# Performance work log

Hardware: AMD Instinct MI355X
Metric: run time of the kernel (lower is better)

Reference implementation:

```python
import jax, jax.numpy as jnp
import numpy as np

N_U = 100000   # num 'u' nodes
N_V = 100000   # num 'v' nodes (destination type)
D = 128        # feature dim
E1 = 3200000   # edges ('u','r1','v')
E2 = 3200000   # edges ('v','r2','v')


def setup_inputs() -> dict:
    key = jax.random.key(0)
    ks = jax.random.split(key, 10)
    inv = 1.0 / np.sqrt(D)
    inv3 = 1.0 / np.sqrt(3 * D)
    return {
        "x_u": jax.random.normal(ks[0], (N_U, D), jnp.float32),
        "x_v": jax.random.normal(ks[1], (N_V, D), jnp.float32),
        "W_r1": jax.random.normal(ks[2], (D, D), jnp.float32) * inv,
        "W_r2": jax.random.normal(ks[3], (D, D), jnp.float32) * inv,
        "W_gate": jax.random.normal(ks[4], (3 * D, 3 * D), jnp.float32) * inv3,
        "b_gate": jnp.zeros((3 * D,), jnp.float32),
        "W_aggr": jax.random.normal(ks[5], (3 * D, D), jnp.float32) * inv3,
        "b_aggr": jnp.zeros((D,), jnp.float32),
        "edge_index_r1": jax.random.randint(ks[6], (2, E1), 0, N_V, dtype=jnp.int64),
        "edge_index_r2": jax.random.randint(ks[7], (2, E2), 0, N_V, dtype=jnp.int64),
    }


def reference(x_u, x_v, W_r1, W_r2, W_gate, b_gate, W_aggr, b_aggr,
              edge_index_r1, edge_index_r2):
    n_v = x_v.shape[0]
    # per-edge-type conv: gather source features, per-relation linear message
    msg1 = x_u[edge_index_r1[0]] @ W_r1   # [E1, D]
    msg2 = x_v[edge_index_r2[0]] @ W_r2   # [E2, D]
    # concat all relations targeting dst 'v' (as in out_dict concatenation)
    msg = jnp.concatenate([msg1, msg2], axis=0)              # [E1+E2, D]
    idx = jnp.concatenate([edge_index_r1[1], edge_index_r2[1]])  # [E1+E2]
    # sum aggregation (scatter_add into zeros of shape [N_v, D])
    s = jax.ops.segment_sum(msg, idx, num_segments=n_v)
    # mean = sum / count.clamp(min=1)
    cnt = jax.ops.segment_sum(jnp.ones_like(msg), idx, num_segments=n_v)
    mean = s / jnp.clip(cnt, 1.0)
    # max with include_self=True over zero-initialized output -> max(msgs, 0), empty rows = 0
    mx = jnp.maximum(jax.ops.segment_max(msg, idx, num_segments=n_v), 0.0)
    total = jnp.concatenate([s, mean, mx], axis=1)           # [N_v, 3D]
    mask = jnp.sum(jnp.abs(total), axis=1) == 0              # untouched nodes
    gate = jax.nn.sigmoid(total @ W_gate + b_gate)           # attention gate
    out = (total * gate) @ W_aggr + b_aggr                   # [N_v, D]
    return jnp.where(mask[:, None], 0.0, out)
```

## Files before the change

### kernel.cpp

```cpp
#include <hip/hip_runtime.h>
#include <math.h>

#define N_U 100000
#define N_V 100000
#define D 128
#define E1 3200000
#define E2 3200000
#define ETOT (E1 + E2)

#define NBUCK 196
#define SLACK 35000
#define PCHUNK 4096

typedef __bf16 bf16x8 __attribute__((ext_vector_type(8)));
typedef float f32x4 __attribute__((ext_vector_type(4)));

__device__ __forceinline__ unsigned short f2b(float f) {
  union { float f; unsigned int u; } v; v.f = f;
  unsigned int u = v.u;
  unsigned int r = u + 0x7fffu + ((u >> 16) & 1u);
  return (unsigned short)(r >> 16);
}
__device__ __forceinline__ float b2f(unsigned short s) {
  union { unsigned int u; float f; } v; v.u = ((unsigned int)s) << 16; return v.f;
}
__device__ __forceinline__ float b2f_lo(unsigned w) {
  union { unsigned u; float f; } v; v.u = w << 16; return v.f;
}
__device__ __forceinline__ float b2f_hi(unsigned w) {
  union { unsigned u; float f; } v; v.u = w & 0xffff0000u; return v.f;
}

__global__ void convert_w128(const float* __restrict__ W, unsigned short* __restrict__ WF) {
  int idx = blockIdx.x * 256 + threadIdx.x;
  if (idx < 128 * 128) {
    int k = idx >> 7, n = idx & 127;
    int f = (n >> 4) * 4 + (k >> 5);
    int out = f * 512 + ((n & 15) + 16 * ((k >> 3) & 3)) * 8 + (k & 7);
    WF[out] = f2b(W[k * 128 + n]);
  }
}
__global__ void convert_wg(const float* __restrict__ Wg, unsigned short* __restrict__ WgF) {
  int idx = blockIdx.x * 256 + threadIdx.x;
  if (idx < 384 * 384) {
    int k = idx / 384, n = idx - k * 384;
    int f = (n >> 4) * 12 + (k >> 5);
    int out = f * 512 + ((n & 15) + 16 * ((k >> 3) & 3)) * 8 + (k & 7);
    WgF[out] = f2b(Wg[k * 384 + n]);
  }
}
__global__ void convert_wa(const float* __restrict__ Wa, unsigned short* __restrict__ WaF) {
  int idx = blockIdx.x * 256 + threadIdx.x;
  if (idx < 384 * 128) {
    int k = idx >> 7, n = idx & 127;
    int f = (n >> 4) * 12 + (k >> 5);
    int out = f * 512 + ((n & 15) + 16 * ((k >> 3) & 3)) * 8 + (k & 7);
    WaF[out] = f2b(Wa[k * 128 + n]);
  }
}

#define LM 64
__global__ __launch_bounds__(256) void linear_mfma(
    const float* __restrict__ X, const unsigned short* __restrict__ WF,
    unsigned short* __restrict__ Hb, int nrows) {
  __shared__ unsigned short Xs[LM][136];
  const int t = threadIdx.x;
  const int row0 = blockIdx.x * LM;

  for (int i = t * 4; i < LM * 128; i += 1024) {
    int n = i >> 7, j = i & 127;
    int r = row0 + n;
    float4 v = make_float4(0.f, 0.f, 0.f, 0.f);
    if (r < nrows) v = *(const float4*)&X[(size_t)r * 128 + j];
    Xs[n][j] = f2b(v.x);
    Xs[n][j + 1] = f2b(v.y);
    Xs[n][j + 2] = f2b(v.z);
    Xs[n][j + 3] = f2b(v.w);
  }
  __syncthreads();

  const int wv = t >> 6;
  const int ln = t & 63;
  const int lr = ln & 15;
  const int lq = ln >> 4;
  const int m0 = wv * 16;

  bf16x8 a[4];
#pragma unroll
  for (int ks = 0; ks < 4; ks++)
    a[ks] = *(const bf16x8*)&Xs[m0 + lr][ks * 32 + lq * 8];

#pragma unroll
  for (int np = 0; np < 4; np++) {
    const int n0 = np * 32;
    f32x4 acc0 = {0.f, 0.f, 0.f, 0.f};
    f32x4 acc1 = {0.f, 0.f, 0.f, 0.f};
    const unsigned short* B0 = WF + (size_t)(np * 2) * 4 * 512 + ln * 8;
    const unsigned short* B1 = B0 + 4 * 512;
#pragma unroll
    for (int ks = 0; ks < 4; ks++) {
      bf16x8 b0 = *(const bf16x8*)(B0 + ks * 512);
      bf16x8 b1 = *(const bf16x8*)(B1 + ks * 512);
      acc0 = __builtin_amdgcn_mfma_f32_16x16x32_bf16(a[ks], b0, acc0, 0, 0, 0);
      acc1 = __builtin_amdgcn_mfma_f32_16x16x32_bf16(a[ks], b1, acc1, 0, 0, 0);
    }
#pragma unroll
    for (int r = 0; r < 4; r++) {
      int grow = row0 + m0 + lq * 4 + r;
      if (grow < nrows) {
        Hb[(size_t)grow * 128 + n0 + lr] = f2b(acc0[r]);
        Hb[(size_t)grow * 128 + n0 + 16 + lr] = f2b(acc1[r]);
      }
    }
  }
}

__global__ __launch_bounds__(256) void partition_kernel(
    const int* __restrict__ e1, const int* __restrict__ e2,
    int* __restrict__ bucketCursor, uint2* __restrict__ recs) {
  __shared__ int hist[256];
  __shared__ int scan_s[256];
  __shared__ int lstart[256];
  __shared__ int gbase[NBUCK];
  __shared__ int lcur[NBUCK];
  __shared__ uint2 buf[PCHUNK];

  const int t = threadIdx.x;
  const long base = (long)blockIdx.x * PCHUNK;
  const int n = (int)min((long)PCHUNK, (long)ETOT - base);

  hist[t] = 0;
  __syncthreads();

  uint2 myrec[PCHUNK / 256];
  int myb[PCHUNK / 256];
  int cnt = 0;
#pragma unroll
  for (int k = 0; k < PCHUNK / 256; k++) {
    int idx = t + k * 256;
    if (idx < n) {
      long i = base + idx;
      int enc, dst;
      if (i < E1) {
        dst = e1[E1 + i];
        enc = N_V + e1[i];
      } else {
        long j = i - E1;
        dst = e2[E2 + j];
        enc = e2[j];
      }
      myrec[cnt] = make_uint2((unsigned)enc, (unsigned)dst);
      int b = dst >> 9;
      myb[cnt] = b;
      atomicAdd(&hist[b], 1);
      cnt++;
    }
  }
  __syncthreads();

  int v = hist[t];
  scan_s[t] = v;
  __syncthreads();
  for (int off = 1; off < 256; off <<= 1) {
    int tmp = (t >= off) ? scan_s[t - off] : 0;
    __syncthreads();
    scan_s[t] += tmp;
    __syncthreads();
  }
  lstart[t] = scan_s[t] - v;
  if (t < NBUCK) {
    gbase[t] = atomicAdd(&bucketCursor[t], v);
    lcur[t] = scan_s[t] - v;
  }
  __syncthreads();

  for (int k = 0; k < cnt; k++) {
    int p = atomicAdd(&lcur[myb[k]], 1);
    buf[p] = myrec[k];
  }
  __syncthreads();

  for (int p = t; p < n; p += 256) {
    uint2 r = buf[p];
    int b = (int)(r.y >> 9);
    recs[(size_t)b * SLACK + gbase[b] + (p - lstart[b])] = r;
  }
}

__global__ __launch_bounds__(256) void bucket_scan(
    const int* __restrict__ bucketCnt, int* __restrict__ bucketBase) {
  __shared__ int s[256];
  const int t = threadIdx.x;
  int v = (t < NBUCK) ? bucketCnt[t] : 0;
  s[t] = v;
  __syncthreads();
  for (int off = 1; off < 256; off <<= 1) {
    int tmp = (t >= off) ? s[t - off] : 0;
    __syncthreads();
    s[t] += tmp;
    __syncthreads();
  }
  if (t < NBUCK) bucketBase[t] = s[t] - v;
  if (t == 255) bucketBase[NBUCK] = s[255];
}

__global__ __launch_bounds__(512) void bucket_fill(
    const uint2* __restrict__ recs, const int* __restrict__ bucketCnt,
    const int* __restrict__ bucketBase, int* __restrict__ row_ptr,
    int* __restrict__ col) {
  __shared__ int hist[512];
  __shared__ int s[512];
  __shared__ int curF[512];
  __shared__ int curB[512];
  const int t = threadIdx.x;
  const int b = blockIdx.x;
  const size_t slack = (size_t)b * SLACK;
  const int n = bucketCnt[b];
  const int outBase = bucketBase[b];
  const int n0 = b << 9;

  hist[t] = 0;
  __syncthreads();
  for (int p = t; p < n; p += 512)
    atomicAdd(&hist[recs[slack + p].y - n0], 1);
  __syncthreads();

  int v = hist[t];
  s[t] = v;
  __syncthreads();
  for (int off = 1; off < 512; off <<= 1) {
    int tmp = (t >= off) ? s[t - off] : 0;
    __syncthreads();
    s[t] += tmp;
    __syncthreads();
  }
  int excl = s[t] - v;
  curF[t] = excl;
  curB[t] = excl + v;
  int nd = n0 + t;
  if (nd < N_V) row_ptr[nd] = outBase + excl;
  if (b == 0 && t == 0) row_ptr[N_V] = ETOT;
  __syncthreads();

  for (int p = t; p < n; p += 512) {
    uint2 r = recs[slack + p];
    int local = r.y - n0;
    int q;
    if (r.x >= (unsigned)N_V) q = atomicSub(&curB[local], 1) - 1;
    else q = atomicAdd(&curF[local], 1);
    col[outBase + q] = (int)(r.x << 8);
  }
}

#define AGG1(w)                                        \
  do {                                                 \
    float lo = b2f_lo(w), hi = b2f_hi(w);              \
    s[2 * q] += lo; s[2 * q + 1] += hi;                \
    m[2 * q] = fmaxf(m[2 * q], lo);                    \
    m[2 * q + 1] = fmaxf(m[2 * q + 1], hi);            \
  } while (0)

__global__ __launch_bounds__(256) void aggregate_kernel(
    const unsigned short* __restrict__ Hb, const int* __restrict__ row_ptr,
    const int* __restrict__ col, unsigned int* __restrict__ SumB,
    unsigned int* __restrict__ MxB) {
  const int node = blockIdx.x * 4 + (threadIdx.x >> 6);
  const int lane = threadIdx.x & 63;
  const int grp = lane >> 4;
  const int fl = lane & 15;
  const int start = row_ptr[node];
  const int end = row_ptr[node + 1];
  const char* Hc = (const char*)Hb;
  const int byteoff = fl * 16;

  float s[8] = {0.f, 0.f, 0.f, 0.f, 0.f, 0.f, 0.f, 0.f};
  float m[8] = {0.f, 0.f, 0.f, 0.f, 0.f, 0.f, 0.f, 0.f};

  int i = start;
  for (; i + 31 < end; i += 32) {
    uint4 v[8];
#pragma unroll
    for (int g = 0; g < 8; g++) {
      int e = i + g * 4 + grp;
      v[g] = *(const uint4*)(Hc + (unsigned)col[e] + byteoff);
    }
#pragma unroll
    for (int g = 0; g < 8; g++) {
      { int q = 0; AGG1(v[g].x); }
      { int q = 1; AGG1(v[g].y); }
      { int q = 2; AGG1(v[g].z); }
      { int q = 3; AGG1(v[g].w); }
    }
  }
  for (; i < end; i += 4) {
    int e = i + grp;
    int ec = e < end ? e : (end - 1);
    uint4 v = *(const uint4*)(Hc + (unsigned)col[ec] + byteoff);
    if (e >= end) { v.x = 0u; v.y = 0u; v.z = 0u; v.w = 0u; }
    { int q = 0; AGG1(v.x); }
    { int q = 1; AGG1(v.y); }
    { int q = 2; AGG1(v.z); }
    { int q = 3; AGG1(v.w); }
  }

#pragma unroll
  for (int k = 0; k < 8; k++) {
    s[k] += __shfl_xor(s[k], 16, 64);
    m[k] = fmaxf(m[k], __shfl_xor(m[k], 16, 64));
    s[k] += __shfl_xor(s[k], 32, 64);
    m[k] = fmaxf(m[k], __shfl_xor(m[k], 32, 64));
  }

  if (lane < 16) {
    uint4 o;
    o.x = (unsigned)f2b(s[0]) | ((unsigned)f2b(s[1]) << 16);
    o.y = (unsigned)f2b(s[2]) | ((unsigned)f2b(s[3]) << 16);
    o.z = (unsigned)f2b(s[4]) | ((unsigned)f2b(s[5]) << 16);
    o.w = (unsigned)f2b(s[6]) | ((unsigned)f2b(s[7]) << 16);
    ((uint4*)SumB)[(size_t)node * 16 + fl] = o;
  } else if (lane < 32) {
    uint4 o;
    o.x = (unsigned)f2b(m[0]) | ((unsigned)f2b(m[1]) << 16);
    o.y = (unsigned)f2b(m[2]) | ((unsigned)f2b(m[3]) << 16);
    o.z = (unsigned)f2b(m[4]) | ((unsigned)f2b(m[5]) << 16);
    o.w = (unsigned)f2b(m[6]) | ((unsigned)f2b(m[7]) << 16);
    ((uint4*)MxB)[(size_t)node * 16 + fl] = o;
  }
}

#define EM 64
__global__ __launch_bounds__(256, 3) void epilogue_mfma(
    const unsigned short* __restrict__ SumB, const unsigned short* __restrict__ MxB,
    const int* __restrict__ row_ptr, const unsigned short* __restrict__ WgF,
    const float* __restrict__ bg, const unsigned short* __restrict__ WaF,
    const float* __restrict__ ba, float* __restrict__ Out) {
  __shared__ unsigned short Ts[EM][392];
  __shared__ float invs[EM];
  __shared__ int cnts[EM];

  const int t = threadIdx.x;
  const int node0 = blockIdx.x * EM;

  if (t < EM) {
    int nd = node0 + t;
    int c = 0;
    if (nd < N_V) c = row_ptr[nd + 1] - row_ptr[nd];
    cnts[t] = c;
    invs[t] = 1.0f / (float)(c > 0 ? c : 1);
  }
  __syncthreads();

  {
    const uint4* Sv = (const uint4*)SumB;
    const uint4* Mv = (const uint4*)MxB;
    for (int i = t; i < EM * 16; i += 256) {
      int n = i >> 4, u = i & 15;
      int nd = node0 + n;
      uint4 s = make_uint4(0u, 0u, 0u, 0u);
      uint4 m4 = make_uint4(0u, 0u, 0u, 0u);
      if (nd < N_V) {
        s = Sv[(size_t)nd * 16 + u];
        m4 = Mv[(size_t)nd * 16 + u];
      }
      float inv = invs[n];
      *(uint4*)&Ts[n][u * 8] = s;
      unsigned sw[4] = {s.x, s.y, s.z, s.w};
      unsigned mr[4];
#pragma unroll
      for (int q = 0; q < 4; q++) {
        unsigned short lo = f2b(b2f((unsigned short)sw[q]) * inv);
        unsigned short hi = f2b(b2f((unsigned short)(sw[q] >> 16)) * inv);
        mr[q] = (unsigned)lo | ((unsigned)hi << 16);
      }
      *(uint4*)&Ts[n][128 + u * 8] = make_uint4(mr[0], mr[1], mr[2], mr[3]);
      *(uint4*)&Ts[n][256 + u * 8] = m4;
    }
  }
  __syncthreads();

  const int wv = t >> 6;
  const int ln = t & 63;
  const int lr = ln & 15;
  const int lq = ln >> 4;

  f32x4 acc[4][6];
#pragma unroll
  for (int m = 0; m < 4; m++)
#pragma unroll
    for (int nt = 0; nt < 6; nt++) acc[m][nt] = (f32x4){0.f, 0.f, 0.f, 0.f};

  const unsigned short* Bg = WgF + (size_t)(wv * 6) * 12 * 512 + ln * 8;

#pragma unroll 2
  for (int kc = 0; kc < 12; kc++) {
    bf16x8 b[6];
#pragma unroll
    for (int nt = 0; nt < 6; nt++)
      b[nt] = *(const bf16x8*)(Bg + (nt * 12 + kc) * 512);
    bf16x8 a[4];
#pragma unroll
    for (int m = 0; m < 4; m++)
      a[m] = *(const bf16x8*)&Ts[m * 16 + lr][kc * 32 + lq * 8];
#pragma unroll
    for (int m = 0; m < 4; m++)
#pragma unroll
      for (int nt = 0; nt < 6; nt++)
        acc[m][nt] = __builtin_amdgcn_mfma_f32_16x16x32_bf16(a[m], b[nt], acc[m][nt], 0, 0, 0);
  }
  __syncthreads();

#pragma unroll
  for (int nt = 0; nt < 6; nt++) {
    int cg = wv * 96 + nt * 16 + lr;
    float bgv = bg[cg];
#pragma unroll
    for (int m = 0; m < 4; m++) {
#pragma unroll
      for (int r = 0; r < 4; r++) {
        int row = m * 16 + lq * 4 + r;
        float g = 1.f / (1.f + __expf(-(acc[m][nt][r] + bgv)));
        Ts[row][cg] = f2b(b2f(Ts[row][cg]) * g);
      }
    }
  }
  __syncthreads();

  f32x4 acc2[4][2];
#pragma unroll
  for (int m = 0; m < 4; m++)
#pragma unroll
    for (int nt = 0; nt < 2; nt++) acc2[m][nt] = (f32x4){0.f, 0.f, 0.f, 0.f};

  const unsigned short* Ba = WaF + (size_t)(wv * 2) * 12 * 512 + ln * 8;

#pragma unroll 2
  for (int kc = 0; kc < 12; kc++) {
    bf16x8 b[2];
#pragma unroll
    for (int nt = 0; nt < 2; nt++)
      b[nt] = *(const bf16x8*)(Ba + (nt * 12 + kc) * 512);
    bf16x8 a[4];
#pragma unroll
    for (int m = 0; m < 4; m++)
      a[m] = *(const bf16x8*)&Ts[m * 16 + lr][kc * 32 + lq * 8];
#pragma unroll
    for (int m = 0; m < 4; m++)
#pragma unroll
      for (int nt = 0; nt < 2; nt++)
        acc2[m][nt] = __builtin_amdgcn_mfma_f32_16x16x32_bf16(a[m], b[nt], acc2[m][nt], 0, 0, 0);
  }

#pragma unroll
  for (int nt = 0; nt < 2; nt++) {
    int cg = wv * 32 + nt * 16 + lr;
    float bav = ba[cg];
#pragma unroll
    for (int m = 0; m < 4; m++) {
#pragma unroll
      for (int r = 0; r < 4; r++) {
        int row = m * 16 + lq * 4 + r;
        int nd = node0 + row;
        if (nd < N_V) {
          float msk = (cnts[row] > 0) ? 1.f : 0.f;
          Out[(size_t)nd * D + cg] = (acc2[m][nt][r] + bav) * msk;
        }
      }
    }
  }
}

extern "C" void kernel_launch(void* const* d_in, const int* in_sizes, int n_in,
                              void* d_out, int out_size, void* d_ws, size_t ws_size,
                              hipStream_t stream) {
  const float* x_u = (const float*)d_in[0];
  const float* x_v = (const float*)d_in[1];
  const float* W_r1 = (const float*)d_in[2];
  const float* W_r2 = (const float*)d_in[3];
  const float* W_gate = (const float*)d_in[4];
  const float* b_gate = (const float*)d_in[5];
  const float* W_aggr = (const float*)d_in[6];
  const float* b_aggr = (const float*)d_in[7];
  const int* e1 = (const int*)d_in[8];
  const int* e2 = (const int*)d_in[9];
  float* out = (float*)d_out;

  char* ws = (char*)d_ws;
  size_t off = 0;
  unsigned short* Hb = (unsigned short*)(ws + off); off += (size_t)(N_V + N_U) * D * 2;
  unsigned int* SumB = (unsigned int*)(ws + off);   off += (size_t)N_V * D * 2;
  unsigned int* MxB = (unsigned int*)(ws + off);    off += (size_t)N_V * D * 2;
  int* colA = (int*)(ws + off);        off += (size_t)ETOT * 4;
  uint2* recs = (uint2*)(ws + off);    off += (size_t)NBUCK * SLACK * 8;
  int* row_ptr = (int*)(ws + off);     off += (size_t)(N_V + 1) * 4;
  int* bucketCursor = (int*)(ws + off); off += NBUCK * 4;
  int* bucketBase = (int*)(ws + off);  off += (NBUCK + 1) * 4;
  unsigned short* Wg16 = (unsigned short*)(ws + off); off += (size_t)384 * 384 * 2;
  unsigned short* Wa16 = (unsigned short*)(ws + off); off += (size_t)128 * 384 * 2;
  unsigned short* Wr1T = (unsigned short*)(ws + off); off += (size_t)128 * 128 * 2;
  unsigned short* Wr2T = (unsigned short*)(ws + off); off += (size_t)128 * 128 * 2;

  hipMemsetAsync(bucketCursor, 0, NBUCK * 4, stream);

  convert_w128<<<64, 256, 0, stream>>>(W_r1, Wr1T);
  convert_w128<<<64, 256, 0, stream>>>(W_r2, Wr2T);
  convert_wg<<<(384 * 384 + 255) / 256, 256, 0, stream>>>(W_gate, Wg16);
  convert_wa<<<(128 * 384 + 255) / 256, 256, 0, stream>>>(W_aggr, Wa16);

  linear_mfma<<<(N_V + LM - 1) / LM, 256, 0, stream>>>(x_v, Wr2T, Hb, N_V);
  linear_mfma<<<(N_U + LM - 1) / LM, 256, 0, stream>>>(x_u, Wr1T, Hb + (size_t)N_V * D, N_U);

  partition_kernel<<<(ETOT + PCHUNK - 1) / PCHUNK, 256, 0, stream>>>(
      e1, e2, bucketCursor, recs);
  bucket_scan<<<1, 256, 0, stream>>>(bucketCursor, bucketBase);
  bucket_fill<<<NBUCK, 512, 0, stream>>>(recs, bucketCursor, bucketBase, row_ptr, colA);

  aggregate_kernel<<<N_V / 4, 256, 0, stream>>>(Hb, row_ptr, colA, SumB, MxB);

  epilogue_mfma<<<(N_V + EM - 1) / EM, 256, 0, stream>>>(
      (const unsigned short*)SumB, (const unsigned short*)MxB, row_ptr,
      Wg16, b_gate, Wa16, b_aggr, out);
}
```

Measured before the change: 657.8 us.

## Merge weight conversions, linear, and partition into fewer launches; fold bucket scan

Combines the four weight-conversion kernels into one launch. It also merges both node linear transforms and the edge partition into a single heterogeneous kernel that uses a shared-memory union. The bucket prefix scan is folded into bucket_fill, where every block recomputes it. Nontemporal loads for col and nontemporal stores for the aggregate outputs are added. The aim is to cut launch overhead and let independent stages overlap, at the cost of larger shared memory per block for the linear blocks and redundant scan work.

```diff
diff --git a/kernel.cpp b/kernel.cpp
--- a/kernel.cpp
+++ b/kernel.cpp
@@ -12,8 +12,13 @@
 #define SLACK 35000
 #define PCHUNK 4096
 
+#define NBL_V 1563
+#define NBL_U 1563
+#define NBL_P 1563
+
 typedef __bf16 bf16x8 __attribute__((ext_vector_type(8)));
 typedef float f32x4 __attribute__((ext_vector_type(4)));
+typedef unsigned int u32x4 __attribute__((ext_vector_type(4)));
 
 __device__ __forceinline__ unsigned short f2b(float f) {
   union { float f; unsigned int u; } v; v.f = f;
@@ -31,51 +36,60 @@
   union { unsigned u; float f; } v; v.u = w & 0xffff0000u; return v.f;
 }
 
-__global__ void convert_w128(const float* __restrict__ W, unsigned short* __restrict__ WF) {
-  int idx = blockIdx.x * 256 + threadIdx.x;
-  if (idx < 128 * 128) {
+__global__ __launch_bounds__(256) void convert_all(
+    const float* __restrict__ W_r1, const float* __restrict__ W_r2,
+    const float* __restrict__ W_gate, const float* __restrict__ W_aggr,
+    unsigned short* __restrict__ Wr1F, unsigned short* __restrict__ Wr2F,
+    unsigned short* __restrict__ WgF, unsigned short* __restrict__ WaF) {
+  const int b = blockIdx.x;
+  if (b < 128) {
+    const float* W = (b < 64) ? W_r1 : W_r2;
+    unsigned short* WF = (b < 64) ? Wr1F : Wr2F;
+    int idx = (b & 63) * 256 + threadIdx.x;
     int k = idx >> 7, n = idx & 127;
     int f = (n >> 4) * 4 + (k >> 5);
     int out = f * 512 + ((n & 15) + 16 * ((k >> 3) & 3)) * 8 + (k & 7);
     WF[out] = f2b(W[k * 128 + n]);
-  }
-}
-__global__ void convert_wg(const float* __restrict__ Wg, unsigned short* __restrict__ WgF) {
-  int idx = blockIdx.x * 256 + threadIdx.x;
-  if (idx < 384 * 384) {
+  } else if (b < 704) {
+    int idx = (b - 128) * 256 + threadIdx.x;
     int k = idx / 384, n = idx - k * 384;
     int f = (n >> 4) * 12 + (k >> 5);
     int out = f * 512 + ((n & 15) + 16 * ((k >> 3) & 3)) * 8 + (k & 7);
-    WgF[out] = f2b(Wg[k * 384 + n]);
-  }
-}
-__global__ void convert_wa(const float* __restrict__ Wa, unsigned short* __restrict__ WaF) {
-  int idx = blockIdx.x * 256 + threadIdx.x;
-  if (idx < 384 * 128) {
+    WgF[out] = f2b(W_gate[k * 384 + n]);
+  } else {
+    int idx = (b - 704) * 256 + threadIdx.x;
     int k = idx >> 7, n = idx & 127;
     int f = (n >> 4) * 12 + (k >> 5);
     int out = f * 512 + ((n & 15) + 16 * ((k >> 3) & 3)) * 8 + (k & 7);
-    WaF[out] = f2b(Wa[k * 128 + n]);
+    WaF[out] = f2b(W_aggr[k * 128 + n]);
   }
 }
 
 #define LM 64
-__global__ __launch_bounds__(256) void linear_mfma(
+union SMem1 {
+  struct { unsigned short Xs[LM][136]; } lin;
+  struct {
+    int hist[256]; int scan_s[256]; int lstart[256];
+    int gbase[NBUCK]; int lcur[NBUCK];
+    uint2 buf[PCHUNK];
+  } part;
+};
+
+__device__ __forceinline__ void do_linear(
     const float* __restrict__ X, const unsigned short* __restrict__ WF,
-    unsigned short* __restrict__ Hb, int nrows) {
-  __shared__ unsigned short Xs[LM][136];
+    unsigned short* __restrict__ Hb, int nrows, int bid, SMem1& sm) {
   const int t = threadIdx.x;
-  const int row0 = blockIdx.x * LM;
+  const int row0 = bid * LM;
 
   for (int i = t * 4; i < LM * 128; i += 1024) {
     int n = i >> 7, j = i & 127;
     int r = row0 + n;
     float4 v = make_float4(0.f, 0.f, 0.f, 0.f);
     if (r < nrows) v = *(const float4*)&X[(size_t)r * 128 + j];
-    Xs[n][j] = f2b(v.x);
-    Xs[n][j + 1] = f2b(v.y);
-    Xs[n][j + 2] = f2b(v.z);
-    Xs[n][j + 3] = f2b(v.w);
+    sm.lin.Xs[n][j] = f2b(v.x);
+    sm.lin.Xs[n][j + 1] = f2b(v.y);
+    sm.lin.Xs[n][j + 2] = f2b(v.z);
+    sm.lin.Xs[n][j + 3] = f2b(v.w);
   }
   __syncthreads();
 
@@ -88,7 +102,7 @@
   bf16x8 a[4];
 #pragma unroll
   for (int ks = 0; ks < 4; ks++)
-    a[ks] = *(const bf16x8*)&Xs[m0 + lr][ks * 32 + lq * 8];
+    a[ks] = *(const bf16x8*)&sm.lin.Xs[m0 + lr][ks * 32 + lq * 8];
 
 #pragma unroll
   for (int np = 0; np < 4; np++) {
@@ -115,21 +129,15 @@
   }
 }
 
-__global__ __launch_bounds__(256) void partition_kernel(
+__device__ __forceinline__ void do_partition(
     const int* __restrict__ e1, const int* __restrict__ e2,
-    int* __restrict__ bucketCursor, uint2* __restrict__ recs) {
-  __shared__ int hist[256];
-  __shared__ int scan_s[256];
-  __shared__ int lstart[256];
-  __shared__ int gbase[NBUCK];
-  __shared__ int lcur[NBUCK];
-  __shared__ uint2 buf[PCHUNK];
-
+    int* __restrict__ bucketCursor, uint2* __restrict__ recs,
+    int bid, SMem1& sm) {
   const int t = threadIdx.x;
-  const long base = (long)blockIdx.x * PCHUNK;
+  const long base = (long)bid * PCHUNK;
   const int n = (int)min((long)PCHUNK, (long)ETOT - base);
 
-  hist[t] = 0;
+  sm.part.hist[t] = 0;
   __syncthreads();
 
   uint2 myrec[PCHUNK / 256];
@@ -152,47 +160,74 @@
       myrec[cnt] = make_uint2((unsigned)enc, (unsigned)dst);
       int b = dst >> 9;
       myb[cnt] = b;
-      atomicAdd(&hist[b], 1);
+      atomicAdd(&sm.part.hist[b], 1);
       cnt++;
     }
   }
   __syncthreads();
 
-  int v = hist[t];
-  scan_s[t] = v;
+  int v = sm.part.hist[t];
+  sm.part.scan_s[t] = v;
   __syncthreads();
   for (int off = 1; off < 256; off <<= 1) {
-    int tmp = (t >= off) ? scan_s[t - off] : 0;
+    int tmp = (t >= off) ? sm.part.scan_s[t - off] : 0;
     __syncthreads();
-    scan_s[t] += tmp;
+    sm.part.scan_s[t] += tmp;
     __syncthreads();
   }
-  lstart[t] = scan_s[t] - v;
+  sm.part.lstart[t] = sm.part.scan_s[t] - v;
   if (t < NBUCK) {
-    gbase[t] = atomicAdd(&bucketCursor[t], v);
-    lcur[t] = scan_s[t] - v;
+    sm.part.gbase[t] = atomicAdd(&bucketCursor[t], v);
+    sm.part.lcur[t] = sm.part.scan_s[t] - v;
   }
   __syncthreads();
 
   for (int k = 0; k < cnt; k++) {
-    int p = atomicAdd(&lcur[myb[k]], 1);
-    buf[p] = myrec[k];
+    int p = atomicAdd(&sm.part.lcur[myb[k]], 1);
+    sm.part.buf[p] = myrec[k];
   }
   __syncthreads();
 
   for (int p = t; p < n; p += 256) {
-    uint2 r = buf[p];
+    uint2 r = sm.part.buf[p];
     int b = (int)(r.y >> 9);
-    recs[(size_t)b * SLACK + gbase[b] + (p - lstart[b])] = r;
-  }
-}
-
-__global__ __launch_bounds__(256) void bucket_scan(
-    const int* __restrict__ bucketCnt, int* __restrict__ bucketBase) {
-  __shared__ int s[256];
+    recs[(size_t)b * SLACK + sm.part.gbase[b] + (p - sm.part.lstart[b])] = r;
+  }
+}
+
+__global__ __launch_bounds__(256) void stage1(
+    const float* __restrict__ x_v, const float* __restrict__ x_u,
+    const unsigned short* __restrict__ Wr2F, const unsigned short* __restrict__ Wr1F,
+    unsigned short* __restrict__ Hb,
+    const int* __restrict__ e1, const int* __restrict__ e2,
+    int* __restrict__ bucketCursor, uint2* __restrict__ recs) {
+  __shared__ SMem1 sm;
+  const int b = blockIdx.x;
+  if (b < NBL_V) {
+    do_linear(x_v, Wr2F, Hb, N_V, b, sm);
+  } else if (b < NBL_V + NBL_U) {
+    do_linear(x_u, Wr1F, Hb + (size_t)N_V * D, N_U, b - NBL_V, sm);
+  } else {
+    do_partition(e1, e2, bucketCursor, recs, b - NBL_V - NBL_U, sm);
+  }
+}
+
+__global__ __launch_bounds__(512) void bucket_fill(
+    const uint2* __restrict__ recs, const int* __restrict__ bucketCnt,
+    int* __restrict__ row_ptr, int* __restrict__ col) {
+  __shared__ int hist[512];
+  __shared__ int s[512];
+  __shared__ int curF[512];
+  __shared__ int curB[512];
+  __shared__ int sh_outBase;
   const int t = threadIdx.x;
-  int v = (t < NBUCK) ? bucketCnt[t] : 0;
-  s[t] = v;
+  const int b = blockIdx.x;
+  const size_t slack = (size_t)b * SLACK;
+  const int n = bucketCnt[b];
+  const int n0 = b << 9;
+
+  int cv = (t < NBUCK) ? bucketCnt[t] : 0;
+  s[t] = cv;
   __syncthreads();
   for (int off = 1; off < 256; off <<= 1) {
     int tmp = (t >= off) ? s[t - off] : 0;
@@ -200,24 +235,9 @@
     s[t] += tmp;
     __syncthreads();
   }
-  if (t < NBUCK) bucketBase[t] = s[t] - v;
-  if (t == 255) bucketBase[NBUCK] = s[255];
-}
-
-__global__ __launch_bounds__(512) void bucket_fill(
-    const uint2* __restrict__ recs, const int* __restrict__ bucketCnt,
-    const int* __restrict__ bucketBase, int* __restrict__ row_ptr,
-    int* __restrict__ col) {
-  __shared__ int hist[512];
-  __shared__ int s[512];
-  __shared__ int curF[512];
-  __shared__ int curB[512];
-  const int t = threadIdx.x;
-  const int b = blockIdx.x;
-  const size_t slack = (size_t)b * SLACK;
-  const int n = bucketCnt[b];
-  const int outBase = bucketBase[b];
-  const int n0 = b << 9;
+  if (t == b) sh_outBase = s[t] - cv;
+  __syncthreads();
+  const int outBase = sh_outBase;
 
   hist[t] = 0;
   __syncthreads();
@@ -282,7 +302,8 @@
 #pragma unroll
     for (int g = 0; g < 8; g++) {
       int e = i + g * 4 + grp;
-      v[g] = *(const uint4*)(Hc + (unsigned)col[e] + byteoff);
+      int cb = __builtin_nontemporal_load(&col[e]);
+      v[g] = *(const uint4*)(Hc + (unsigned)cb + byteoff);
     }
 #pragma unroll
     for (int g = 0; g < 8; g++) {
@@ -295,7 +316,8 @@
   for (; i < end; i += 4) {
     int e = i + grp;
     int ec = e < end ? e : (end - 1);
-    uint4 v = *(const uint4*)(Hc + (unsigned)col[ec] + byteoff);
+    int cb = __builtin_nontemporal_load(&col[ec]);
+    uint4 v = *(const uint4*)(Hc + (unsigned)cb + byteoff);
     if (e >= end) { v.x = 0u; v.y = 0u; v.z = 0u; v.w = 0u; }
     { int q = 0; AGG1(v.x); }
     { int q = 1; AGG1(v.y); }
@@ -312,19 +334,19 @@
   }
 
   if (lane < 16) {
-    uint4 o;
+    u32x4 o;
     o.x = (unsigned)f2b(s[0]) | ((unsigned)f2b(s[1]) << 16);
     o.y = (unsigned)f2b(s[2]) | ((unsigned)f2b(s[3]) << 16);
     o.z = (unsigned)f2b(s[4]) | ((unsigned)f2b(s[5]) << 16);
     o.w = (unsigned)f2b(s[6]) | ((unsigned)f2b(s[7]) << 16);
-    ((uint4*)SumB)[(size_t)node * 16 + fl] = o;
+    __builtin_nontemporal_store(o, (u32x4*)SumB + (size_t)node * 16 + fl);
   } else if (lane < 32) {
-    uint4 o;
+    u32x4 o;
     o.x = (unsigned)f2b(m[0]) | ((unsigned)f2b(m[1]) << 16);
     o.y = (unsigned)f2b(m[2]) | ((unsigned)f2b(m[3]) << 16);
     o.z = (unsigned)f2b(m[4]) | ((unsigned)f2b(m[5]) << 16);
     o.w = (unsigned)f2b(m[6]) | ((unsigned)f2b(m[7]) << 16);
-    ((uint4*)MxB)[(size_t)node * 16 + fl] = o;
+    __builtin_nontemporal_store(o, (u32x4*)MxB + (size_t)node * 16 + fl);
   }
 }
 
@@ -501,18 +523,13 @@
 
   hipMemsetAsync(bucketCursor, 0, NBUCK * 4, stream);
 
-  convert_w128<<<64, 256, 0, stream>>>(W_r1, Wr1T);
-  convert_w128<<<64, 256, 0, stream>>>(W_r2, Wr2T);
-  convert_wg<<<(384 * 384 + 255) / 256, 256, 0, stream>>>(W_gate, Wg16);
-  convert_wa<<<(128 * 384 + 255) / 256, 256, 0, stream>>>(W_aggr, Wa16);
-
-  linear_mfma<<<(N_V + LM - 1) / LM, 256, 0, stream>>>(x_v, Wr2T, Hb, N_V);
-  linear_mfma<<<(N_U + LM - 1) / LM, 256, 0, stream>>>(x_u, Wr1T, Hb + (size_t)N_V * D, N_U);
-
-  partition_kernel<<<(ETOT + PCHUNK - 1) / PCHUNK, 256, 0, stream>>>(
-      e1, e2, bucketCursor, recs);
-  bucket_scan<<<1, 256, 0, stream>>>(bucketCursor, bucketBase);
-  bucket_fill<<<NBUCK, 512, 0, stream>>>(recs, bucketCursor, bucketBase, row_ptr, colA);
+  convert_all<<<896, 256, 0, stream>>>(W_r1, W_r2, W_gate, W_aggr,
+                                       Wr1T, Wr2T, Wg16, Wa16);
+
+  stage1<<<NBL_V + NBL_U + NBL_P, 256, 0, stream>>>(
+      x_v, x_u, Wr2T, Wr1T, Hb, e1, e2, bucketCursor, recs);
+
+  bucket_fill<<<NBUCK, 512, 0, stream>>>(recs, bucketCursor, row_ptr, colA);
 
   aggregate_kernel<<<N_V / 4, 256, 0, stream>>>(Hb, row_ptr, colA, SumB, MxB);
 
```

Measured after the change: 661.8 us. Within noise of the previous version (+0.6%).
